# Optimization experiments

Measured on AMD Instinct MI355X. Metric: run time of the kernel, lower is better.

Reference implementation:

```python
import jax, jax.numpy as jnp
import numpy as np

POOL = 7          # cf.pool_size
SR = 2            # roi_align sampling_ratio
LEVELS = [0, 1, 2, 3]
C = 192           # cf.end_filts
HC = 2            # cf.head_classes
RF = 1
N_ROIS = 1000
B = 4


def roi_align_2d(fmap, boxes, batch_inds, pool_size=POOL, sr=SR):
    """Bilinear RoIAlign. fmap [B,C,H,W]; boxes [N,4] = (y1,x1,y2,x2) in fmap pixel coords."""
    _, _, H, W = fmap.shape
    y1, x1, y2, x2 = boxes[:, 0], boxes[:, 1], boxes[:, 2], boxes[:, 3]
    bin_h = jnp.maximum(y2 - y1, 1.0) / pool_size
    bin_w = jnp.maximum(x2 - x1, 1.0) / pool_size
    # sampling offsets within the roi, [pool*sr]
    grid = (jnp.arange(pool_size, dtype=jnp.float32)[:, None]
            + (jnp.arange(sr, dtype=jnp.float32)[None, :] + 0.5) / sr).reshape(-1)
    ys = y1[:, None] + grid[None, :] * bin_h[:, None]   # [N, P*S]
    xs = x1[:, None] + grid[None, :] * bin_w[:, None]   # [N, P*S]
    y = jnp.broadcast_to(ys[:, :, None], (ys.shape[0], ys.shape[1], xs.shape[1]))  # [N,PS,PS]
    x = jnp.broadcast_to(xs[:, None, :], y.shape)
    valid = (y >= -1.0) & (y <= H) & (x >= -1.0) & (x <= W)
    y = jnp.clip(y, 0.0, H - 1)
    x = jnp.clip(x, 0.0, W - 1)
    y0 = jnp.floor(y).astype(jnp.int32)
    x0 = jnp.floor(x).astype(jnp.int32)
    y1i = jnp.minimum(y0 + 1, H - 1)
    x1i = jnp.minimum(x0 + 1, W - 1)
    ly = y - y0
    lx = x - x0
    b = batch_inds[:, None, None]
    f00 = fmap[b, :, y0, x0]    # [N,PS,PS,C]
    f01 = fmap[b, :, y0, x1i]
    f10 = fmap[b, :, y1i, x0]
    f11 = fmap[b, :, y1i, x1i]
    w00 = ((1 - ly) * (1 - lx))[..., None]
    w01 = ((1 - ly) * lx)[..., None]
    w10 = (ly * (1 - lx))[..., None]
    w11 = (ly * lx)[..., None]
    val = (f00 * w00 + f01 * w01 + f10 * w10 + f11 * w11) * valid[..., None]
    n = val.shape[0]
    val = val.reshape(n, pool_size, sr, pool_size, sr, -1).mean(axis=(2, 4))  # [N,P,P,C]
    return jnp.transpose(val, (0, 3, 1, 2))  # [N,C,P,P]


def pyramid_roi_align(fmaps, rois, pool_size=POOL, levels=LEVELS):
    boxes = jax.lax.stop_gradient(rois[:, :4])  # level_boxes.detach() in original
    batch_ix = rois[:, 4].astype(jnp.int32)
    h = boxes[:, 2] - boxes[:, 0]
    w = boxes[:, 3] - boxes[:, 1]
    roi_level = jnp.clip(jnp.round(4.0 + jnp.log2(jnp.sqrt(h * w))),
                         levels[0], levels[-1]).astype(jnp.int32)
    pooled = jnp.zeros((boxes.shape[0], fmaps[0].shape[1], pool_size, pool_size), fmaps[0].dtype)
    for li, lvl in enumerate(levels):
        H, W = fmaps[li].shape[2], fmaps[li].shape[3]
        scale = jnp.asarray([H, W, H, W], jnp.float32)
        p = roi_align_2d(fmaps[li], boxes * scale, batch_ix, pool_size)
        pooled = jnp.where((roi_level == lvl)[:, None, None, None], p, pooled)
    return pooled


def setup_inputs() -> dict:
    key = jax.random.key(0)
    ks = jax.random.split(key, 20)
    fmap0 = jax.random.normal(ks[0], (B, C, 128, 128), jnp.float32)
    fmap1 = jax.random.normal(ks[1], (B, C, 64, 64), jnp.float32)
    fmap2 = jax.random.normal(ks[2], (B, C, 32, 32), jnp.float32)
    fmap3 = jax.random.normal(ks[3], (B, C, 16, 16), jnp.float32)
    # valid normalized rois: (y1,x1,y2,x2,batch_ix)
    cy = jax.random.uniform(ks[4], (N_ROIS,), minval=0.15, maxval=0.85)
    cx = jax.random.uniform(ks[5], (N_ROIS,), minval=0.15, maxval=0.85)
    hh = jax.random.uniform(ks[6], (N_ROIS,), minval=0.02, maxval=0.15)
    hw = jax.random.uniform(ks[7], (N_ROIS,), minval=0.02, maxval=0.15)
    bix = jax.random.randint(ks[8], (N_ROIS,), 0, B).astype(jnp.float32)
    rois = jnp.stack([jnp.clip(cy - hh, 0, 1), jnp.clip(cx - hw, 0, 1),
                      jnp.clip(cy + hh, 0, 1), jnp.clip(cx + hw, 0, 1), bix], axis=1)
    d = C * 4  # 768
    s1 = 1.0 / np.sqrt(C * POOL * POOL)
    s2 = 1.0 / np.sqrt(d)
    params = dict(
        w1=jax.random.normal(ks[9], (d, C, POOL, POOL), jnp.float32) * s1,
        b1=jnp.zeros((d,), jnp.float32),
        w2=jax.random.normal(ks[10], (d, d), jnp.float32) * s2,
        b2=jnp.zeros((d,), jnp.float32),
        w_bbox=jax.random.normal(ks[11], (HC * 4, d), jnp.float32) * s2,
        b_bbox=jnp.zeros((HC * 4,), jnp.float32),
        w_cls=jax.random.normal(ks[12], (HC, d), jnp.float32) * s2,
        b_cls=jnp.zeros((HC,), jnp.float32),
        w_reg=jax.random.normal(ks[13], (HC * RF, d), jnp.float32) * s2,
        b_reg=jnp.zeros((HC * RF,), jnp.float32),
        w_unc=jax.random.normal(ks[14], (HC, d), jnp.float32) * s2,
        b_unc=jnp.zeros((HC,), jnp.float32),
    )
    return dict(fmap0=fmap0, fmap1=fmap1, fmap2=fmap2, fmap3=fmap3, rois=rois, **params)


def reference(fmap0, fmap1, fmap2, fmap3, rois, w1, b1, w2, b2,
              w_bbox, b_bbox, w_cls, b_cls, w_reg, b_reg, w_unc, b_unc):
    x = pyramid_roi_align([fmap0, fmap1, fmap2, fmap3], rois)      # [N,C,7,7]
    x = jax.nn.relu(jnp.einsum('ncij,ocij->no', x, w1) + b1)       # conv1 ks=7 -> 1x1
    x = jax.nn.relu(x @ w2.T + b2)                                 # conv2 1x1
    n = x.shape[0]
    mrcnn_bbox = (x @ w_bbox.T + b_bbox).reshape(n, -1, 4)         # [N,HC,2*dim]
    mrcnn_class_logits = x @ w_cls.T + b_cls                       # [N,HC]
    reg = (x @ w_reg.T + b_reg).reshape(n, -1, RF)
    unc = x @ w_unc.T + b_unc
    mrcnn_regress = jnp.concatenate([reg, unc[..., None]], axis=2)  # [N,HC,RF+1]
    return mrcnn_bbox, mrcnn_class_logits, mrcnn_regress
```

## Files before the change

### kernel.cpp

```cpp
#include <hip/hip_runtime.h>
#include <hip/hip_bf16.h>
#include <cstddef>
#include <cstdint>

typedef __attribute__((ext_vector_type(8))) short short8;
typedef __attribute__((ext_vector_type(16))) float float16;

#define C_CH 192
#define PK   9408
#define D1   768

__device__ __forceinline__ ushort f2bf(float v) {
    return __builtin_bit_cast(unsigned short, __float2bfloat16(v));
}
__device__ __forceinline__ float bf2f(ushort u) {
    return __builtin_bit_cast(float, ((unsigned int)u) << 16);
}

__global__ __launch_bounds__(256) void cvt_bf16_2(
    const float* __restrict__ in1, ushort* __restrict__ out1, int n4_1,
    const float* __restrict__ in2, ushort* __restrict__ out2, int n4_2)
{
    int i = blockIdx.x * 256 + threadIdx.x;
    const float* in; ushort* out;
    if (i < n4_1) { in = in1; out = out1; }
    else          { i -= n4_1; if (i >= n4_2) return; in = in2; out = out2; }
    float4 v = ((const float4*)in)[i];
    ushort4 o;
    o.x = f2bf(v.x); o.y = f2bf(v.y); o.z = f2bf(v.z); o.w = f2bf(v.w);
    ((ushort4*)out)[i] = o;
}

__global__ __launch_bounds__(256) void cvt_bf16(const float* __restrict__ in,
                                                ushort* __restrict__ out, int n4)
{
    int i = blockIdx.x * 256 + threadIdx.x;
    if (i >= n4) return;
    float4 v = ((const float4*)in)[i];
    ushort4 o;
    o.x = f2bf(v.x); o.y = f2bf(v.y); o.z = f2bf(v.z); o.w = f2bf(v.w);
    ((ushort4*)out)[i] = o;
}

__global__ __launch_bounds__(256) void nchw_to_nhwc(
    const float* __restrict__ f0, const float* __restrict__ f1,
    const float* __restrict__ f2, const float* __restrict__ f3,
    ushort* __restrict__ o0, ushort* __restrict__ o1,
    ushort* __restrict__ o2, ushort* __restrict__ o3)
{
    __shared__ float sm[C_CH][33];
    int t = blockIdx.x;
    int b = blockIdx.y;
    const float* in; ushort* out; int HW, hw0;
    if      (t < 512) { in = f0; out = o0; HW = 16384; hw0 = t * 32; }
    else if (t < 640) { in = f1; out = o1; HW = 4096;  hw0 = (t - 512) * 32; }
    else if (t < 672) { in = f2; out = o2; HW = 1024;  hw0 = (t - 640) * 32; }
    else              { in = f3; out = o3; HW = 256;   hw0 = (t - 672) * 32; }

    int tx = threadIdx.x & 31;
    int ty = threadIdx.x >> 5;

    const float* ip = in + (size_t)b * C_CH * HW + hw0;
    #pragma unroll
    for (int c = 0; c < C_CH; c += 8)
        sm[c + ty][tx] = ip[(size_t)(c + ty) * HW + tx];
    __syncthreads();

    ushort* op = out + ((size_t)b * HW + hw0) * C_CH;
    #pragma unroll
    for (int r0 = 0; r0 < 32; r0 += 8) {
        int r = r0 + ty;
        #pragma unroll
        for (int cc = 0; cc < 6; ++cc) {
            int c = cc * 32 + tx;
            op[(size_t)r * C_CH + c] = f2bf(sm[c][r]);
        }
    }
}

__global__ __launch_bounds__(384) void roi_gather(
    const ushort* __restrict__ n0p, const ushort* __restrict__ n1p,
    const ushort* __restrict__ n2p, const ushort* __restrict__ n3p,
    const float* __restrict__ rois, ushort* __restrict__ pooled)
{
    __shared__ int   s_offB[196][4];
    __shared__ float s_w[196][4];
    __shared__ ushort s_out[PK];

    const int n   = blockIdx.x;
    const int tid = threadIdx.x;

    float by1 = rois[n*5+0], bx1 = rois[n*5+1];
    float by2 = rois[n*5+2], bx2 = rois[n*5+3];
    int   b   = (int)rois[n*5+4];

    float hh = by2 - by1, ww = bx2 - bx1;
    int lvl = (int)rintf(4.0f + log2f(sqrtf(hh * ww)));
    lvl = min(max(lvl, 0), 3);

    const ushort* fm; int H;
    if      (lvl == 0) { fm = n0p; H = 128; }
    else if (lvl == 1) { fm = n1p; H = 64;  }
    else if (lvl == 2) { fm = n2p; H = 32;  }
    else               { fm = n3p; H = 16;  }
    float Hf = (float)H;

    float y1p = by1 * Hf, x1p = bx1 * Hf;
    float y2p = by2 * Hf, x2p = bx2 * Hf;
    float bin_h = fmaxf(y2p - y1p, 1.0f) * (1.0f / 7.0f);
    float bin_w = fmaxf(x2p - x1p, 1.0f) * (1.0f / 7.0f);

    uintptr_t bp = (uintptr_t)(fm + (size_t)b * H * H * C_CH);
    unsigned int blo = __builtin_amdgcn_readfirstlane((unsigned int)bp);
    unsigned int bhi = __builtin_amdgcn_readfirstlane((unsigned int)(bp >> 32));
    const char* sbase = (const char*)((((uintptr_t)bhi) << 32) | blo);

    if (tid < 196) {
        int s  = tid;
        int sx = s & 1, sy = (s >> 1) & 1, ij = s >> 2;
        int i = ij / 7, j = ij - i * 7;

        float gy = (float)i + 0.25f + 0.5f * (float)sy;
        float y  = y1p + gy * bin_h;
        bool  vy = (y >= -1.0f) && (y <= Hf);
        float yc = fminf(fmaxf(y, 0.0f), Hf - 1.0f);
        int   y0 = (int)floorf(yc);
        float ly = yc - (float)y0;
        int   y1i = min(y0 + 1, H - 1);

        float gx = (float)j + 0.25f + 0.5f * (float)sx;
        float x  = x1p + gx * bin_w;
        bool  vx = (x >= -1.0f) && (x <= Hf);
        float xc = fminf(fmaxf(x, 0.0f), Hf - 1.0f);
        int   x0 = (int)floorf(xc);
        float lx = xc - (float)x0;
        int   x1i = min(x0 + 1, H - 1);

        float vm = (vy && vx) ? 0.25f : 0.0f;
        s_offB[s][0] = (y0  * H + x0 ) * (C_CH * 2);
        s_offB[s][1] = (y0  * H + x1i) * (C_CH * 2);
        s_offB[s][2] = (y1i * H + x0 ) * (C_CH * 2);
        s_offB[s][3] = (y1i * H + x1i) * (C_CH * 2);
        s_w[s][0] = (1.0f - ly) * (1.0f - lx) * vm;
        s_w[s][1] = (1.0f - ly) * lx * vm;
        s_w[s][2] = ly * (1.0f - lx) * vm;
        s_w[s][3] = ly * lx * vm;
    }
    __syncthreads();

    const int grp = tid / 96;
    const int ci  = tid - grp * 96;
    const int c   = ci * 2;
    const int c4  = ci * 4;
    const int bin_lo = grp * 13;
    const int bin_hi = min(bin_lo + 13, 49);

    for (int bin = bin_lo; bin < bin_hi; ++bin) {
        float a0 = 0.0f, a1 = 0.0f;
        #pragma unroll
        for (int sub = 0; sub < 4; ++sub) {
            int s = bin * 4 + sub;
            #pragma unroll
            for (int tp = 0; tp < 4; ++tp) {
                int ob  = s_offB[s][tp];
                float w = s_w[s][tp];
                unsigned int u = *(const unsigned int*)(sbase + (ob + c4));
                float lo = __builtin_bit_cast(float, u << 16);
                float hi = __builtin_bit_cast(float, u & 0xffff0000u);
                a0 = fmaf(lo, w, a0);
                a1 = fmaf(hi, w, a1);
            }
        }
        s_out[(c + 0) * 49 + bin] = f2bf(a0);
        s_out[(c + 1) * 49 + bin] = f2bf(a1);
    }
    __syncthreads();

    unsigned int* po = (unsigned int*)(pooled + (size_t)n * PK);
    const unsigned int* so = (const unsigned int*)s_out;
    for (int idx = tid; idx < PK / 2; idx += 384) po[idx] = so[idx];
}

__global__ __launch_bounds__(256) void roi_align_nchw(
    const float* __restrict__ f0, const float* __restrict__ f1,
    const float* __restrict__ f2, const float* __restrict__ f3,
    const float* __restrict__ rois, ushort* __restrict__ pooled, int n_rois)
{
    int idx = blockIdx.x * 256 + threadIdx.x;
    if (idx >= n_rois * PK) return;
    int n  = idx / PK;
    int r  = idx - n * PK;
    int c  = r / 49;
    int ij = r - c * 49;
    int i  = ij / 7;
    int j  = ij - i * 7;

    float by1 = rois[n*5+0], bx1 = rois[n*5+1];
    float by2 = rois[n*5+2], bx2 = rois[n*5+3];
    int   b   = (int)rois[n*5+4];

    float hh = by2 - by1, ww = bx2 - bx1;
    int lvl = (int)rintf(4.0f + log2f(sqrtf(hh * ww)));
    lvl = min(max(lvl, 0), 3);

    const float* fmap; int H;
    if      (lvl == 0) { fmap = f0; H = 128; }
    else if (lvl == 1) { fmap = f1; H = 64;  }
    else if (lvl == 2) { fmap = f2; H = 32;  }
    else               { fmap = f3; H = 16;  }
    float Hf = (float)H;

    float y1p = by1 * Hf, x1p = bx1 * Hf;
    float bin_h = fmaxf(by2 * Hf - y1p, 1.0f) * (1.0f / 7.0f);
    float bin_w = fmaxf(bx2 * Hf - x1p, 1.0f) * (1.0f / 7.0f);

    const float* base = fmap + ((size_t)b * C_CH + c) * (size_t)(H * H);

    float acc = 0.0f;
    #pragma unroll
    for (int sy = 0; sy < 2; ++sy) {
        float y  = y1p + ((float)i + 0.25f + 0.5f * (float)sy) * bin_h;
        bool  vy = (y >= -1.0f) && (y <= Hf);
        float yc = fminf(fmaxf(y, 0.0f), Hf - 1.0f);
        int   y0 = (int)floorf(yc);
        float ly = yc - (float)y0;
        int   y1i = min(y0 + 1, H - 1);
        #pragma unroll
        for (int sx = 0; sx < 2; ++sx) {
            float x  = x1p + ((float)j + 0.25f + 0.5f * (float)sx) * bin_w;
            bool  vx = (x >= -1.0f) && (x <= Hf);
            float xc = fminf(fmaxf(x, 0.0f), Hf - 1.0f);
            int   x0 = (int)floorf(xc);
            float lx = xc - (float)x0;
            int   x1i = min(x0 + 1, H - 1);
            if (vy && vx) {
                float v = base[y0 * H + x0 ] * (1.0f - ly) * (1.0f - lx)
                        + base[y0 * H + x1i] * (1.0f - ly) * lx
                        + base[y1i * H + x0 ] * ly * (1.0f - lx)
                        + base[y1i * H + x1i] * ly * lx;
                acc += v;
            }
        }
    }
    pooled[idx] = f2bf(acc * 0.25f);
}

template<int MODE>
__global__ __launch_bounds__(256) void mfma_gemm(
    const ushort* __restrict__ A, const ushort* __restrict__ W,
    const float* __restrict__ bias, void* __restrict__ outp,
    int M, int N, int K, int nkPer, int nkTotal)
{
    __shared__ char ldsA[2][8192];
    __shared__ char ldsB[2][8192];

    const int t    = threadIdx.x;
    const int lane = t & 63;
    const int wave = t >> 6;
    const int wm = wave >> 1, wn = wave & 1;

    const int m0 = blockIdx.y * 64;
    const int n0 = blockIdx.x * 64;
    const int kb = (MODE == 2) ? blockIdx.z * nkPer : 0;
    const int nk = (MODE == 2) ? min(nkPer, nkTotal - kb) : nkPer;

    const int ks   = t & 3;
    const int mrow = t >> 2;
    const int g    = mrow >> 5;
    const int rw   = mrow & 31;
    const int lof0 = ks*2048 + g*1024 + ((     rw) ^ (ks<<2))*16;
    const int lof1 = ks*2048 + g*1024 + ((32 + rw) ^ (ks<<2))*16;

    const int arow = min(m0 + mrow, M-1);
    const int brow = n0 + mrow;
    const ushort* ap = A + (size_t)arow * K + (size_t)kb * 64 + ks*16;
    const ushort* bp = W + (size_t)brow * K + (size_t)kb * 64 + ks*16;

    float4 ra0, ra1, rb0, rb1;
    float4 qa0, qa1, qb0, qb1;

    ra0 = ((const float4*)ap)[0]; ra1 = ((const float4*)ap)[1];
    rb0 = ((const float4*)bp)[0]; rb1 = ((const float4*)bp)[1];
    *(float4*)&ldsA[0][lof0] = ra0; *(float4*)&ldsA[0][lof1] = ra1;
    *(float4*)&ldsB[0][lof0] = rb0; *(float4*)&ldsB[0][lof1] = rb1;
    {
        int k1 = min(1, nk - 1);
        const ushort* ap1 = ap + (size_t)k1 * 64;
        const ushort* bp1 = bp + (size_t)k1 * 64;
        ra0 = ((const float4*)ap1)[0]; ra1 = ((const float4*)ap1)[1];
        rb0 = ((const float4*)bp1)[0]; rb1 = ((const float4*)bp1)[1];
    }
    __syncthreads();

    float16 acc = {};

    for (int kt = 0; kt < nk; ++kt) {
        {
            int k2 = min(kt + 2, nk - 1);
            const ushort* ap2 = ap + (size_t)k2 * 64;
            const ushort* bp2 = bp + (size_t)k2 * 64;
            qa0 = ((const float4*)ap2)[0]; qa1 = ((const float4*)ap2)[1];
            qb0 = ((const float4*)bp2)[0]; qb1 = ((const float4*)bp2)[1];
        }
        if (kt + 1 < nk) {
            char* dA = ldsA[(kt+1)&1]; char* dB = ldsB[(kt+1)&1];
            *(float4*)&dA[lof0] = ra0; *(float4*)&dA[lof1] = ra1;
            *(float4*)&dB[lof0] = rb0; *(float4*)&dB[lof1] = rb1;
        }
        const char* sA = ldsA[kt&1]; const char* sB = ldsB[kt&1];
        #pragma unroll
        for (int s = 0; s < 4; ++s) {
            int ro = s*2048 + (lane ^ (s<<2))*16;
            short8 af = *(const short8*)&sA[wm*1024 + ro];
            short8 bf = *(const short8*)&sB[wn*1024 + ro];
            acc = __builtin_amdgcn_mfma_f32_32x32x16_bf16(af, bf, acc, 0, 0, 0);
        }
        __syncthreads();
        ra0 = qa0; ra1 = qa1; rb0 = qb0; rb1 = qb1;
    }

    const int col   = lane & 31;
    const int rbase = 4 * (lane >> 5);
    const int nG    = n0 + wn*32 + col;

    if (MODE == 2) {
        float* O = (float*)outp + (size_t)blockIdx.z * M * N;
        #pragma unroll
        for (int r = 0; r < 16; ++r) {
            int row = (r & 3) + 8*(r >> 2) + rbase;
            int mG  = m0 + wm*32 + row;
            if (mG < M) O[(size_t)mG * N + nG] = acc[r];
        }
    } else if (MODE == 1) {
        const float bv = bias[nG];
        ushort* O = (ushort*)outp;
        #pragma unroll
        for (int r = 0; r < 16; ++r) {
            int row = (r & 3) + 8*(r >> 2) + rbase;
            int mG  = m0 + wm*32 + row;
            if (mG < M) O[(size_t)mG * N + nG] = f2bf(fmaxf(acc[r] + bv, 0.0f));
        }
    } else {
        const float bv = bias[nG];
        float* O = (float*)outp;
        #pragma unroll
        for (int r = 0; r < 16; ++r) {
            int row = (r & 3) + 8*(r >> 2) + rbase;
            int mG  = m0 + wm*32 + row;
            if (mG < M) O[(size_t)mG * N + nG] = fmaxf(acc[r] + bv, 0.0f);
        }
    }
}

__global__ __launch_bounds__(256) void reduce_relu_bf16(
    const float* __restrict__ P, const float* __restrict__ bias,
    ushort* __restrict__ Y, int MN, int N, int S)
{
    int idx = blockIdx.x * 256 + threadIdx.x;
    if (idx >= MN / 4) return;
    float4 s = ((const float4*)P)[idx];
    for (int k = 1; k < S; ++k) {
        float4 p = ((const float4*)(P + (size_t)k * MN))[idx];
        s.x += p.x; s.y += p.y; s.z += p.z; s.w += p.w;
    }
    int n4 = idx % (N / 4);
    float4 bv = ((const float4*)bias)[n4];
    ushort4 o;
    o.x = f2bf(fmaxf(s.x + bv.x, 0.0f));
    o.y = f2bf(fmaxf(s.y + bv.y, 0.0f));
    o.z = f2bf(fmaxf(s.z + bv.z, 0.0f));
    o.w = f2bf(fmaxf(s.w + bv.w, 0.0f));
    ((ushort4*)Y)[idx] = o;
}

__global__ __launch_bounds__(256) void reduce_heads(
    const float* __restrict__ P2, const float* __restrict__ b2, int S, int MN,
    const float* __restrict__ w_bbox, const float* __restrict__ b_bbox,
    const float* __restrict__ w_cls,  const float* __restrict__ b_cls,
    const float* __restrict__ w_reg,  const float* __restrict__ b_reg,
    const float* __restrict__ w_unc,  const float* __restrict__ b_unc,
    float* __restrict__ out, int n_rois)
{
    __shared__ float zrow[D1];
    const int m   = blockIdx.x;
    const int tid = threadIdx.x;

    const float* Pm = P2 + (size_t)m * D1;
    #pragma unroll
    for (int r = 0; r < 3; ++r) {
        int k = r * 256 + tid;
        float v = Pm[k];
        for (int s = 1; s < S; ++s) v += Pm[(size_t)s * MN + k];
        zrow[k] = fmaxf(v + b2[k], 0.0f);
    }
    __syncthreads();

    const int wave = tid >> 6;
    const int lane = tid & 63;
    for (int o = wave; o < 14; o += 4) {
        const float* w; float bb;
        if      (o < 8)  { w = w_bbox + o * D1;        bb = b_bbox[o]; }
        else if (o < 10) { w = w_cls  + (o - 8) * D1;  bb = b_cls[o - 8]; }
        else if (o < 12) { w = w_reg  + (o - 10) * D1; bb = b_reg[o - 10]; }
        else             { w = w_unc  + (o - 12) * D1; bb = b_unc[o - 12]; }
        float p = 0.0f;
        #pragma unroll
        for (int r = 0; r < 12; ++r) {
            int k = r * 64 + lane;
            p = fmaf(zrow[k], w[k], p);
        }
        #pragma unroll
        for (int d = 32; d >= 1; d >>= 1) p += __shfl_down(p, d, 64);
        if (lane == 0) {
            int off;
            int clsOff = n_rois * 8;
            int regOff = n_rois * 10;
            if      (o < 8)  off = m * 8 + o;
            else if (o < 10) off = clsOff + m * 2 + (o - 8);
            else if (o < 12) off = regOff + m * 4 + (o - 10) * 2;
            else             off = regOff + m * 4 + (o - 12) * 2 + 1;
            out[off] = p + bb;
        }
    }
}

__global__ __launch_bounds__(256) void heads_kernel(
    const float* __restrict__ Z,
    const float* __restrict__ w_bbox, const float* __restrict__ b_bbox,
    const float* __restrict__ w_cls,  const float* __restrict__ b_cls,
    const float* __restrict__ w_reg,  const float* __restrict__ b_reg,
    const float* __restrict__ w_unc,  const float* __restrict__ b_unc,
    float* __restrict__ out, int n_rois)
{
    int idx = blockIdx.x * 256 + threadIdx.x;
    if (idx >= n_rois * 14) return;
    int n = idx / 14;
    int o = idx - n * 14;

    const float* w; float bb;
    if      (o < 8)  { w = w_bbox + o * D1;        bb = b_bbox[o]; }
    else if (o < 10) { w = w_cls  + (o - 8) * D1;  bb = b_cls[o - 8]; }
    else if (o < 12) { w = w_reg  + (o - 10) * D1; bb = b_reg[o - 10]; }
    else             { w = w_unc  + (o - 12) * D1; bb = b_unc[o - 12]; }

    const float* z = Z + (size_t)n * D1;
    float s = bb;
    for (int k = 0; k < D1; k += 4) {
        float4 zv = *(const float4*)(z + k);
        float4 wv = *(const float4*)(w + k);
        s = fmaf(zv.x, wv.x, s);
        s = fmaf(zv.y, wv.y, s);
        s = fmaf(zv.z, wv.z, s);
        s = fmaf(zv.w, wv.w, s);
    }

    int off;
    int clsOff = n_rois * 8;
    int regOff = n_rois * 10;
    if      (o < 8)  off = n * 8 + o;
    else if (o < 10) off = clsOff + n * 2 + (o - 8);
    else if (o < 12) off = regOff + n * 4 + (o - 10) * 2;
    else             off = regOff + n * 4 + (o - 12) * 2 + 1;
    out[off] = s;
}

extern "C" void kernel_launch(void* const* d_in, const int* in_sizes, int n_in,
                              void* d_out, int out_size, void* d_ws, size_t ws_size,
                              hipStream_t stream)
{
    const float* f0   = (const float*)d_in[0];
    const float* f1   = (const float*)d_in[1];
    const float* f2   = (const float*)d_in[2];
    const float* f3   = (const float*)d_in[3];
    const float* rois = (const float*)d_in[4];
    const float* w1   = (const float*)d_in[5];
    const float* b1   = (const float*)d_in[6];
    const float* w2   = (const float*)d_in[7];
    const float* b2   = (const float*)d_in[8];
    const float* w_bbox = (const float*)d_in[9];
    const float* b_bbox = (const float*)d_in[10];
    const float* w_cls  = (const float*)d_in[11];
    const float* b_cls  = (const float*)d_in[12];
    const float* w_reg  = (const float*)d_in[13];
    const float* b_reg  = (const float*)d_in[14];
    const float* w_unc  = (const float*)d_in[15];
    const float* b_unc  = (const float*)d_in[16];
    float* out = (float*)d_out;

    const int n_rois = in_sizes[4] / 5;
    const int B      = in_sizes[0] / (C_CH * 128 * 128);

    const size_t nh0B = (size_t)B * 16384 * C_CH * 2;
    const size_t nh1B = (size_t)B * 4096  * C_CH * 2;
    const size_t nh2B = (size_t)B * 1024  * C_CH * 2;
    const size_t nh3B = (size_t)B * 256   * C_CH * 2;
    const size_t nhAll = nh0B + nh1B + nh2B + nh3B;
    const size_t poolB = (size_t)n_rois * PK * 2;
    const size_t w1Bb  = (size_t)D1 * PK * 2;
    const size_t w2Bb  = (size_t)D1 * D1 * 2;
    const size_t Yb    = (size_t)n_rois * D1 * 2;
    const size_t Zb    = (size_t)n_rois * D1 * 4;
    const size_t smallB = w2Bb + Yb + Zb;

    const size_t needX = nhAll + poolB + smallB;

    char* ws = (char*)d_ws;

    if (ws_size >= needX) {
        const int SPLIT1 = 5;
        const int SPLIT2 = 2;

        ushort* nh0 = (ushort*)ws;
        ushort* nh1 = nh0 + nh0B/2;
        ushort* nh2 = nh1 + nh1B/2;
        ushort* nh3 = nh2 + nh2B/2;
        ushort* w1B = (ushort*)ws;
        float*  P   = (float*)(ws + w1Bb);
        float*  P2  = (float*)ws;
        ushort* pooledB = (ushort*)(ws + nhAll);
        ushort* w2B = (ushort*)(ws + nhAll + poolB);
        ushort* Y   = w2B + w2Bb/2;

        nchw_to_nhwc<<<dim3(680, B), 256, 0, stream>>>(f0, f1, f2, f3,
                                                       nh0, nh1, nh2, nh3);
        roi_gather<<<n_rois, 384, 0, stream>>>(nh0, nh1, nh2, nh3, rois, pooledB);

        {
            int n41 = D1*PK/4, n42 = D1*D1/4;
            cvt_bf16_2<<<(n41 + n42 + 255)/256, 256, 0, stream>>>(
                w1, w1B, n41, w2, w2B, n42);
        }
        {
            int nkTotal = PK / 64;
            int nkPer   = (nkTotal + SPLIT1 - 1) / SPLIT1;
            dim3 grid(D1/64, (n_rois + 63)/64, SPLIT1);
            mfma_gemm<2><<<grid, 256, 0, stream>>>(pooledB, w1B, nullptr, P,
                                                   n_rois, D1, PK, nkPer, nkTotal);
            int MN = n_rois * D1;
            reduce_relu_bf16<<<(MN/4 + 255)/256, 256, 0, stream>>>(P, b1, Y, MN, D1, SPLIT1);
        }
        {
            int nkTotal = D1 / 64;
            int nkPer   = nkTotal / SPLIT2;
            dim3 grid(D1/64, (n_rois + 63)/64, SPLIT2);
            mfma_gemm<2><<<grid, 256, 0, stream>>>(Y, w2B, nullptr, P2,
                                                   n_rois, D1, D1, nkPer, nkTotal);
            int MN = n_rois * D1;
            reduce_heads<<<n_rois, 256, 0, stream>>>(P2, b2, SPLIT2, MN,
                w_bbox, b_bbox, w_cls, b_cls, w_reg, b_reg, w_unc, b_unc, out, n_rois);
        }
    } else {
        ushort* pooledB = (ushort*)ws;
        ushort* w1B = pooledB + poolB/2;
        ushort* w2B = w1B + w1Bb/2;
        ushort* Y   = w2B + w2Bb/2;
        float*  Z   = (float*)((char*)Y + Yb);

        cvt_bf16<<<((D1*PK/4) + 255)/256, 256, 0, stream>>>(w1, w1B, D1*PK/4);
        cvt_bf16<<<((D1*D1/4) + 255)/256, 256, 0, stream>>>(w2, w2B, D1*D1/4);
        {
            int total = n_rois * PK;
            roi_align_nchw<<<(total + 255)/256, 256, 0, stream>>>(
                f0, f1, f2, f3, rois, pooledB, n_rois);
        }
        {
            dim3 grid(D1/64, (n_rois + 63)/64);
            mfma_gemm<1><<<grid, 256, 0, stream>>>(pooledB, w1B, b1, Y,
                                                   n_rois, D1, PK, PK/64, PK/64);
        }
        {
            dim3 grid(D1/64, (n_rois + 63)/64);
            mfma_gemm<0><<<grid, 256, 0, stream>>>(Y, w2B, b2, Z,
                                                   n_rois, D1, D1, D1/64, D1/64);
        }
        heads_kernel<<<(n_rois*14 + 255)/256, 256, 0, stream>>>(
            Z, w_bbox, b_bbox, w_cls, b_cls, w_reg, b_reg, w_unc, b_unc, out, n_rois);
    }
}
```

Before: 246.2 us.

## Stage RoI footprint in LDS, add wider-N fc1 GEMM, flat workspace layout

The RoI gather now copies each RoI's bounding footprint of NHWC cells into shared memory when it fits in 192 cells, then does the bilinear taps from LDS instead of global memory. Offsets and weights are packed into one int2 array. A new fc1 GEMM kernel uses 64x128 tiles with two MFMA accumulators per wave to reuse the A tile across more columns. A non-aliased workspace layout is used when the workspace is large enough, avoiding overlap of w1/P with the NHWC buffers. In exchange, the larger LDS footprint may lower occupancy, and the LDS path is skipped for large RoIs.

```diff
diff --git a/kernel.cpp b/kernel.cpp
--- a/kernel.cpp
+++ b/kernel.cpp
@@ -9,6 +9,7 @@
 #define C_CH 192
 #define PK   9408
 #define D1   768
+#define MAXCELLS 192
 
 __device__ __forceinline__ ushort f2bf(float v) {
     return __builtin_bit_cast(unsigned short, __float2bfloat16(v));
@@ -83,9 +84,9 @@
     const ushort* __restrict__ n2p, const ushort* __restrict__ n3p,
     const float* __restrict__ rois, ushort* __restrict__ pooled)
 {
-    __shared__ int   s_offB[196][4];
-    __shared__ float s_w[196][4];
+    __shared__ ushort s_cells[MAXCELLS * C_CH];
     __shared__ ushort s_out[PK];
+    __shared__ int2   s_ow[196][4];
 
     const int n   = blockIdx.x;
     const int tid = threadIdx.x;
@@ -114,6 +115,19 @@
     unsigned int blo = __builtin_amdgcn_readfirstlane((unsigned int)bp);
     unsigned int bhi = __builtin_amdgcn_readfirstlane((unsigned int)(bp >> 32));
     const char* sbase = (const char*)((((uintptr_t)bhi) << 32) | blo);
+
+    float yA = fminf(fmaxf(y1p + 0.25f * bin_h, 0.0f), Hf - 1.0f);
+    float yB = fminf(fmaxf(y1p + 6.75f * bin_h, 0.0f), Hf - 1.0f);
+    float xA = fminf(fmaxf(x1p + 0.25f * bin_w, 0.0f), Hf - 1.0f);
+    float xB = fminf(fmaxf(x1p + 6.75f * bin_w, 0.0f), Hf - 1.0f);
+    int y_lo = (int)floorf(yA);
+    int y_hi = min((int)floorf(yB) + 1, H - 1);
+    int x_lo = (int)floorf(xA);
+    int x_hi = min((int)floorf(xB) + 1, H - 1);
+    int ey = y_hi - y_lo + 1;
+    int ex = x_hi - x_lo + 1;
+    int cells = ey * ex;
+    bool useLds = (cells <= MAXCELLS);
 
     if (tid < 196) {
         int s  = tid;
@@ -137,14 +151,41 @@
         int   x1i = min(x0 + 1, H - 1);
 
         float vm = (vy && vx) ? 0.25f : 0.0f;
-        s_offB[s][0] = (y0  * H + x0 ) * (C_CH * 2);
-        s_offB[s][1] = (y0  * H + x1i) * (C_CH * 2);
-        s_offB[s][2] = (y1i * H + x0 ) * (C_CH * 2);
-        s_offB[s][3] = (y1i * H + x1i) * (C_CH * 2);
-        s_w[s][0] = (1.0f - ly) * (1.0f - lx) * vm;
-        s_w[s][1] = (1.0f - ly) * lx * vm;
-        s_w[s][2] = ly * (1.0f - lx) * vm;
-        s_w[s][3] = ly * lx * vm;
+        float w0 = (1.0f - ly) * (1.0f - lx) * vm;
+        float w1 = (1.0f - ly) * lx * vm;
+        float w2 = ly * (1.0f - lx) * vm;
+        float w3 = ly * lx * vm;
+
+        int o0, o1, o2, o3;
+        if (useLds) {
+            o0 = ((y0  - y_lo) * ex + (x0  - x_lo)) * (C_CH * 2);
+            o1 = ((y0  - y_lo) * ex + (x1i - x_lo)) * (C_CH * 2);
+            o2 = ((y1i - y_lo) * ex + (x0  - x_lo)) * (C_CH * 2);
+            o3 = ((y1i - y_lo) * ex + (x1i - x_lo)) * (C_CH * 2);
+        } else {
+            o0 = (y0  * H + x0 ) * (C_CH * 2);
+            o1 = (y0  * H + x1i) * (C_CH * 2);
+            o2 = (y1i * H + x0 ) * (C_CH * 2);
+            o3 = (y1i * H + x1i) * (C_CH * 2);
+        }
+        s_ow[s][0] = make_int2(o0, __builtin_bit_cast(int, w0));
+        s_ow[s][1] = make_int2(o1, __builtin_bit_cast(int, w1));
+        s_ow[s][2] = make_int2(o2, __builtin_bit_cast(int, w2));
+        s_ow[s][3] = make_int2(o3, __builtin_bit_cast(int, w3));
+    }
+
+    if (useLds) {
+        int rowDw = ex * 96;
+        int totDw = cells * 96;
+        const unsigned int* src = (const unsigned int*)sbase;
+        unsigned int* dst = (unsigned int*)s_cells;
+        int srcRow0 = (y_lo * H + x_lo) * 96;
+        int rowStride = H * 96;
+        for (int tix = tid; tix < totDw; tix += 384) {
+            int cy = tix / rowDw;
+            int d  = tix - cy * rowDw;
+            dst[tix] = src[srcRow0 + cy * rowStride + d];
+        }
     }
     __syncthreads();
 
@@ -155,24 +196,42 @@
     const int bin_lo = grp * 13;
     const int bin_hi = min(bin_lo + 13, 49);
 
-    for (int bin = bin_lo; bin < bin_hi; ++bin) {
-        float a0 = 0.0f, a1 = 0.0f;
-        #pragma unroll
-        for (int sub = 0; sub < 4; ++sub) {
-            int s = bin * 4 + sub;
+    if (useLds) {
+        for (int bin = bin_lo; bin < bin_hi; ++bin) {
+            float a0 = 0.0f, a1 = 0.0f;
             #pragma unroll
-            for (int tp = 0; tp < 4; ++tp) {
-                int ob  = s_offB[s][tp];
-                float w = s_w[s][tp];
-                unsigned int u = *(const unsigned int*)(sbase + (ob + c4));
-                float lo = __builtin_bit_cast(float, u << 16);
-                float hi = __builtin_bit_cast(float, u & 0xffff0000u);
-                a0 = fmaf(lo, w, a0);
-                a1 = fmaf(hi, w, a1);
+            for (int sub = 0; sub < 4; ++sub) {
+                int s = bin * 4 + sub;
+                #pragma unroll
+                for (int tp = 0; tp < 4; ++tp) {
+                    int2 ow = s_ow[s][tp];
+                    float w = __builtin_bit_cast(float, ow.y);
+                    unsigned int u = *(const unsigned int*)((const char*)s_cells + ow.x + c4);
+                    a0 = fmaf(__builtin_bit_cast(float, u << 16), w, a0);
+                    a1 = fmaf(__builtin_bit_cast(float, u & 0xffff0000u), w, a1);
+                }
             }
-        }
-        s_out[(c + 0) * 49 + bin] = f2bf(a0);
-        s_out[(c + 1) * 49 + bin] = f2bf(a1);
+            s_out[(c + 0) * 49 + bin] = f2bf(a0);
+            s_out[(c + 1) * 49 + bin] = f2bf(a1);
+        }
+    } else {
+        for (int bin = bin_lo; bin < bin_hi; ++bin) {
+            float a0 = 0.0f, a1 = 0.0f;
+            #pragma unroll
+            for (int sub = 0; sub < 4; ++sub) {
+                int s = bin * 4 + sub;
+                #pragma unroll
+                for (int tp = 0; tp < 4; ++tp) {
+                    int2 ow = s_ow[s][tp];
+                    float w = __builtin_bit_cast(float, ow.y);
+                    unsigned int u = *(const unsigned int*)(sbase + ow.x + c4);
+                    a0 = fmaf(__builtin_bit_cast(float, u << 16), w, a0);
+                    a1 = fmaf(__builtin_bit_cast(float, u & 0xffff0000u), w, a1);
+                }
+            }
+            s_out[(c + 0) * 49 + bin] = f2bf(a0);
+            s_out[(c + 1) * 49 + bin] = f2bf(a1);
+        }
     }
     __syncthreads();
 
@@ -348,6 +407,102 @@
             int row = (r & 3) + 8*(r >> 2) + rbase;
             int mG  = m0 + wm*32 + row;
             if (mG < M) O[(size_t)mG * N + nG] = fmaxf(acc[r] + bv, 0.0f);
+        }
+    }
+}
+
+__global__ __launch_bounds__(256) void mfma_gemm_fc1(
+    const ushort* __restrict__ A, const ushort* __restrict__ W,
+    float* __restrict__ P, int M, int N, int K, int nkPer, int nkTotal)
+{
+    __shared__ char ldsA[2][8192];
+    __shared__ char ldsB[2][16384];
+
+    const int t    = threadIdx.x;
+    const int lane = t & 63;
+    const int wave = t >> 6;
+    const int wm = wave >> 1, wn = wave & 1;
+
+    const int m0 = blockIdx.y * 64;
+    const int n0 = blockIdx.x * 128;
+    const int kb = blockIdx.z * nkPer;
+    const int nk = min(nkPer, nkTotal - kb);
+
+    const int ks   = t & 3;
+    const int mrow = t >> 2;
+    const int g0   = mrow >> 5;
+    const int rw   = mrow & 31;
+    const int swz  = ks << 2;
+    const int slot = (rw ^ swz) * 16;
+    const int lofA  = ks*2048 + g0*1024 + slot;
+    const int lofB0 = ks*4096 + g0*1024 + slot;
+    const int lofB1 = ks*4096 + (g0+2)*1024 + slot;
+
+    const int arow = min(m0 + mrow, M-1);
+    const ushort* ap  = A + (size_t)arow * K + (size_t)kb * 64 + ks*16;
+    const ushort* bp0 = W + (size_t)(n0 + mrow)      * K + (size_t)kb * 64 + ks*16;
+    const ushort* bp1 = W + (size_t)(n0 + mrow + 64) * K + (size_t)kb * 64 + ks*16;
+
+    float4 ra0, ra1, rb00, rb01, rb10, rb11;
+    float4 qa0, qa1, qb00, qb01, qb10, qb11;
+
+    ra0  = ((const float4*)ap)[0];  ra1  = ((const float4*)ap)[1];
+    rb00 = ((const float4*)bp0)[0]; rb01 = ((const float4*)bp0)[1];
+    rb10 = ((const float4*)bp1)[0]; rb11 = ((const float4*)bp1)[1];
+    *(float4*)&ldsA[0][lofA]        = ra0;  *(float4*)&ldsA[0][lofA + 512]  = ra1;
+    *(float4*)&ldsB[0][lofB0]       = rb00; *(float4*)&ldsB[0][lofB0 + 512] = rb01;
+    *(float4*)&ldsB[0][lofB1]       = rb10; *(float4*)&ldsB[0][lofB1 + 512] = rb11;
+    {
+        int k1 = min(1, nk - 1);
+        size_t o = (size_t)k1 * 64;
+        ra0  = ((const float4*)(ap  + o))[0]; ra1  = ((const float4*)(ap  + o))[1];
+        rb00 = ((const float4*)(bp0 + o))[0]; rb01 = ((const float4*)(bp0 + o))[1];
+        rb10 = ((const float4*)(bp1 + o))[0]; rb11 = ((const float4*)(bp1 + o))[1];
+    }
+    __syncthreads();
+
+    float16 acc0 = {}, acc1 = {};
+
+    for (int kt = 0; kt < nk; ++kt) {
+        {
+            int k2 = min(kt + 2, nk - 1);
+            size_t o = (size_t)k2 * 64;
+            qa0  = ((const float4*)(ap  + o))[0]; qa1  = ((const float4*)(ap  + o))[1];
+            qb00 = ((const float4*)(bp0 + o))[0]; qb01 = ((const float4*)(bp0 + o))[1];
+            qb10 = ((const float4*)(bp1 + o))[0]; qb11 = ((const float4*)(bp1 + o))[1];
+        }
+        if (kt + 1 < nk) {
+            char* dA = ldsA[(kt+1)&1]; char* dB = ldsB[(kt+1)&1];
+            *(float4*)&dA[lofA]        = ra0;  *(float4*)&dA[lofA + 512]  = ra1;
+            *(float4*)&dB[lofB0]       = rb00; *(float4*)&dB[lofB0 + 512] = rb01;
+            *(float4*)&dB[lofB1]       = rb10; *(float4*)&dB[lofB1 + 512] = rb11;
+        }
+        const char* sA = ldsA[kt&1]; const char* sB = ldsB[kt&1];
+        #pragma unroll
+        for (int s = 0; s < 4; ++s) {
+            int sl = (lane ^ (s<<2)) * 16;
+            short8 af = *(const short8*)&sA[s*2048 + wm*1024 + sl];
+            short8 b0 = *(const short8*)&sB[s*4096 + (wn*2 + 0)*1024 + sl];
+            short8 b1 = *(const short8*)&sB[s*4096 + (wn*2 + 1)*1024 + sl];
+            acc0 = __builtin_amdgcn_mfma_f32_32x32x16_bf16(af, b0, acc0, 0, 0, 0);
+            acc1 = __builtin_amdgcn_mfma_f32_32x32x16_bf16(af, b1, acc1, 0, 0, 0);
+        }
+        __syncthreads();
+        ra0 = qa0; ra1 = qa1;
+        rb00 = qb00; rb01 = qb01; rb10 = qb10; rb11 = qb11;
+    }
+
+    float* O = P + (size_t)blockIdx.z * M * N;
+    const int col   = lane & 31;
+    const int rbase = 4 * (lane >> 5);
+    #pragma unroll
+    for (int r = 0; r < 16; ++r) {
+        int row = (r & 3) + 8*(r >> 2) + rbase;
+        int mG  = m0 + wm*32 + row;
+        if (mG < M) {
+            int nG = n0 + wn*64 + col;
+            O[(size_t)mG * N + nG]      = acc0[r];
+            O[(size_t)mG * N + nG + 32] = acc1[r];
         }
     }
 }
@@ -500,26 +655,39 @@
     const size_t w2Bb  = (size_t)D1 * D1 * 2;
     const size_t Yb    = (size_t)n_rois * D1 * 2;
     const size_t Zb    = (size_t)n_rois * D1 * 4;
-    const size_t smallB = w2Bb + Yb + Zb;
-
-    const size_t needX = nhAll + poolB + smallB;
+
+    const int SPLIT1 = 5;
+    const int SPLIT2 = 2;
+    const size_t Pb  = (size_t)SPLIT1 * n_rois * D1 * 4;
+    const size_t P2b = (size_t)SPLIT2 * n_rois * D1 * 4;
+
+    const size_t needFlat = nhAll + poolB + w1Bb + w2Bb + Yb + Pb + P2b;
+    const size_t needX    = nhAll + poolB + w2Bb + Yb + Zb;
 
     char* ws = (char*)d_ws;
 
-    if (ws_size >= needX) {
-        const int SPLIT1 = 5;
-        const int SPLIT2 = 2;
+    if (ws_size >= needFlat || ws_size >= needX) {
+        const bool flat = (ws_size >= needFlat);
 
         ushort* nh0 = (ushort*)ws;
         ushort* nh1 = nh0 + nh0B/2;
         ushort* nh2 = nh1 + nh1B/2;
         ushort* nh3 = nh2 + nh2B/2;
-        ushort* w1B = (ushort*)ws;
-        float*  P   = (float*)(ws + w1Bb);
-        float*  P2  = (float*)ws;
         ushort* pooledB = (ushort*)(ws + nhAll);
         ushort* w2B = (ushort*)(ws + nhAll + poolB);
         ushort* Y   = w2B + w2Bb/2;
+
+        ushort* w1B; float *P, *P2;
+        if (flat) {
+            char* p = (char*)Y + Yb;
+            w1B = (ushort*)p;          p += w1Bb;
+            P   = (float*)p;           p += Pb;
+            P2  = (float*)p;
+        } else {
+            w1B = (ushort*)ws;
+            P   = (float*)(ws + w1Bb);
+            P2  = (float*)ws;
+        }
 
         nchw_to_nhwc<<<dim3(680, B), 256, 0, stream>>>(f0, f1, f2, f3,
                                                        nh0, nh1, nh2, nh3);
@@ -533,9 +701,9 @@
         {
             int nkTotal = PK / 64;
             int nkPer   = (nkTotal + SPLIT1 - 1) / SPLIT1;
-            dim3 grid(D1/64, (n_rois + 63)/64, SPLIT1);
-            mfma_gemm<2><<<grid, 256, 0, stream>>>(pooledB, w1B, nullptr, P,
-                                                   n_rois, D1, PK, nkPer, nkTotal);
+            dim3 grid(D1/128, (n_rois + 63)/64, SPLIT1);
+            mfma_gemm_fc1<<<grid, 256, 0, stream>>>(pooledB, w1B, P,
+                                                    n_rois, D1, PK, nkPer, nkTotal);
             int MN = n_rois * D1;
             reduce_relu_bf16<<<(MN/4 + 255)/256, 256, 0, stream>>>(P, b1, Y, MN, D1, SPLIT1);
         }
```

Result: slower. 276.3 us (+12.3%).
